# Optimization experiments

Hardware: AMD Instinct MI355X
Metric: run time of the kernel (lower is better)

Reference implementation:

```python
import jax, jax.numpy as jnp
import numpy as np

L = 19
PAD1 = L // 2          # 9 (top/left)
PAD2 = L // 2          # 9 (bottom/right, l is odd)


def setup_inputs() -> dict:
    key = jax.random.key(0)
    k1, k2 = jax.random.split(key)
    B, C, H, W = 2, 3, 256, 256
    inp = jax.random.normal(k1, (B, C, H, W), dtype=jnp.float32)
    # per-pixel blur kernels: (B, H*W, l, l), nonnegative
    kern = jax.random.uniform(k2, (B, H * W, L, L), dtype=jnp.float32)
    return {"input": inp, "kernel": kern}


def reference(input, kernel):
    B, C, H, W = input.shape
    l = L
    K2 = l * l
    # reflection pad (pad_1 left/top, pad_2 right/bottom)
    pad = jnp.pad(input, ((0, 0), (0, 0), (PAD1, PAD2), (PAD1, PAD2)), mode="reflect")
    Hp, Wp = pad.shape[-2:]
    # im2col: (B*C, 1, Hp, Wp) -> (B*C, K2, H, W); with 1 input channel the
    # patch-channel ordering is row-major over (ki, kj), matching torch.Unfold
    x = pad.reshape(B * C, 1, Hp, Wp)
    patches = jax.lax.conv_general_dilated_patches(
        x, filter_shape=(l, l), window_strides=(1, 1), padding="VALID"
    )  # (B*C, K2, H, W)
    patches = patches.reshape(B, C, K2, H * W)
    # kernel: (B, HW, l, l) -> (B, HW, K2); shared across the C=3 channels
    kflat = kernel.reshape(B, H * W, K2)
    # per-pixel weighted sum over the K2 window, then divide by l^2 (divisor_=True)
    out = jnp.einsum("bckp,bpk->bcp", patches, kflat) / jnp.float32(l * l)
    return out.reshape(B, C, H, W)
```

## Files before the change

### kernel.cpp

```cpp
#include <hip/hip_runtime.h>

#define KL   19
#define K2   361
#define W    256
#define H    256
#define HW   65536
#define C    3
#define PADL 9
#define B    2
#define TC   34
#define TPOS (KL * TC)

__global__ __launch_bounds__(256, 8) void blur_fused(
    const float* __restrict__ in,
    const float* __restrict__ kern,
    float* __restrict__ out)
{
    __shared__ float tile[TPOS * 4];

    const int tid = threadIdx.x;
    const int pb  = blockIdx.x << 4;
    const int b   = pb >> 16;
    const int i   = (pb >> 8) & 255;
    const int j0  = pb & 255;

    const float* in_b = in + (size_t)b * (C * HW);
    for (int s = tid; s < TPOS * 4; s += 256) {
        const int ch  = s & 3;
        const int pos = s >> 2;
        if (ch < 3) {
            const int r  = pos / TC;
            const int cc = pos - r * TC;
            int ro = i + r - PADL;
            ro = (ro < 0) ? -ro : ro;
            ro = (ro > H - 1) ? 2 * (H - 1) - ro : ro;
            int co = j0 + cc - PADL;
            co = (co < 0) ? -co : co;
            co = (co > W - 1) ? 2 * (W - 1) - co : co;
            tile[s] = in_b[ch * HW + ro * W + co];
        }
    }
    __syncthreads();

    const int sub = tid & 15;
    const int q   = tid >> 4;
    const int p   = pb + q;
    const float* krow = kern + (size_t)p * K2 + sub;

    float w[23];
    #pragma unroll
    for (int c = 0; c < 23; ++c) {
        const int t = sub + 16 * c;
        w[c] = (t < K2) ? krow[16 * c] : 0.f;
    }

    float a0 = 0.f, a1 = 0.f, a2 = 0.f;
    #pragma unroll
    for (int c = 0; c < 23; ++c) {
        int t = sub + 16 * c;
        if (t > K2 - 1) t = K2 - 1;
        const int ki  = t / KL;
        const int kj  = t - ki * KL;
        const int pos = ki * TC + kj + q;
        const float* src = &tile[pos * 4];
        a0 += w[c] * src[0];
        a1 += w[c] * src[1];
        a2 += w[c] * src[2];
    }

    #pragma unroll
    for (int o = 8; o >= 1; o >>= 1) {
        a0 += __shfl_xor(a0, o, 16);
        a1 += __shfl_xor(a1, o, 16);
        a2 += __shfl_xor(a2, o, 16);
    }

    if (sub == 0) {
        const float s = 1.0f / (float)K2;
        float* ob = out + (size_t)b * (C * HW) + i * W + j0 + q;
        ob[0]      = a0 * s;
        ob[HW]     = a1 * s;
        ob[2 * HW] = a2 * s;
    }
}

extern "C" void kernel_launch(void* const* d_in, const int* in_sizes, int n_in,
                              void* d_out, int out_size, void* d_ws, size_t ws_size,
                              hipStream_t stream) {
    const float* in   = (const float*)d_in[0];
    const float* kern = (const float*)d_in[1];
    float* out        = (float*)d_out;

    const int npix = B * HW;
    dim3 grid(npix / 16), block(256);
    hipLaunchKernelGGL(blur_fused, grid, block, 0, stream, in, kern, out);
}
```

Measured before the change: 38.12 us.

## Process 4x16 pixel tile per block to reuse shared input halo

Each block now covers 4 rows by 16 columns instead of a single 16-pixel row segment, loading a 22x34 halo tile once and looping over the four rows. This cuts the redundant input halo loads, since the old layout reloaded 19 rows per 16 pixels. The grid shrinks by four and each block does four times the work. The kernel weights (the dominant traffic) are still streamed once per pixel, so the gain is limited to halo traffic and fewer block launches, at the cost of fewer blocks to hide latency.

New measurement: 39.13 us. +2.7%, slower.

```diff
diff --git a/kernel.cpp b/kernel.cpp
--- a/kernel.cpp
+++ b/kernel.cpp
@@ -9,7 +9,8 @@
 #define PADL 9
 #define B    2
 #define TC   34
-#define TPOS (KL * TC)
+#define TR   22
+#define TPOS (TR * TC)
 
 __global__ __launch_bounds__(256, 8) void blur_fused(
     const float* __restrict__ in,
@@ -19,10 +20,11 @@
     __shared__ float tile[TPOS * 4];
 
     const int tid = threadIdx.x;
-    const int pb  = blockIdx.x << 4;
-    const int b   = pb >> 16;
-    const int i   = (pb >> 8) & 255;
-    const int j0  = pb & 255;
+    const int bid = blockIdx.x;
+    const int b   = bid >> 10;
+    const int rem = bid & 1023;
+    const int i0  = (rem >> 4) << 2;
+    const int j0  = (rem & 15) << 4;
 
     const float* in_b = in + (size_t)b * (C * HW);
     for (int s = tid; s < TPOS * 4; s += 256) {
@@ -31,7 +33,7 @@
         if (ch < 3) {
             const int r  = pos / TC;
             const int cc = pos - r * TC;
-            int ro = i + r - PADL;
+            int ro = i0 + r - PADL;
             ro = (ro < 0) ? -ro : ro;
             ro = (ro > H - 1) ? 2 * (H - 1) - ro : ro;
             int co = j0 + cc - PADL;
@@ -44,43 +46,46 @@
 
     const int sub = tid & 15;
     const int q   = tid >> 4;
-    const int p   = pb + q;
-    const float* krow = kern + (size_t)p * K2 + sub;
-
-    float w[23];
-    #pragma unroll
-    for (int c = 0; c < 23; ++c) {
-        const int t = sub + 16 * c;
-        w[c] = (t < K2) ? krow[16 * c] : 0.f;
-    }
-
-    float a0 = 0.f, a1 = 0.f, a2 = 0.f;
-    #pragma unroll
-    for (int c = 0; c < 23; ++c) {
-        int t = sub + 16 * c;
-        if (t > K2 - 1) t = K2 - 1;
-        const int ki  = t / KL;
-        const int kj  = t - ki * KL;
-        const int pos = ki * TC + kj + q;
-        const float* src = &tile[pos * 4];
-        a0 += w[c] * src[0];
-        a1 += w[c] * src[1];
-        a2 += w[c] * src[2];
-    }
+    const float scale = 1.0f / (float)K2;
 
     #pragma unroll
-    for (int o = 8; o >= 1; o >>= 1) {
-        a0 += __shfl_xor(a0, o, 16);
-        a1 += __shfl_xor(a1, o, 16);
-        a2 += __shfl_xor(a2, o, 16);
-    }
+    for (int r = 0; r < 4; ++r) {
+        const int p = (i0 + r) * W + j0 + q;
+        const float* krow = kern + ((size_t)b * HW + p) * K2 + sub;
 
-    if (sub == 0) {
-        const float s = 1.0f / (float)K2;
-        float* ob = out + (size_t)b * (C * HW) + i * W + j0 + q;
-        ob[0]      = a0 * s;
-        ob[HW]     = a1 * s;
-        ob[2 * HW] = a2 * s;
+        float w[23];
+        #pragma unroll
+        for (int c = 0; c < 23; ++c) {
+            const int t = sub + 16 * c;
+            w[c] = (t < K2) ? krow[16 * c] : 0.f;
+        }
+
+        float a0 = 0.f, a1 = 0.f, a2 = 0.f;
+        #pragma unroll
+        for (int c = 0; c < 23; ++c) {
+            int t = sub + 16 * c;
+            if (t > K2 - 1) t = K2 - 1;
+            const int ki = t / KL;
+            const int kj = t - ki * KL;
+            const float* src = &tile[((ki + r) * TC + kj + q) * 4];
+            a0 += w[c] * src[0];
+            a1 += w[c] * src[1];
+            a2 += w[c] * src[2];
+        }
+
+        #pragma unroll
+        for (int o = 8; o >= 1; o >>= 1) {
+            a0 += __shfl_xor(a0, o, 16);
+            a1 += __shfl_xor(a1, o, 16);
+            a2 += __shfl_xor(a2, o, 16);
+        }
+
+        if (sub == 0) {
+            float* ob = out + (size_t)b * (C * HW) + p;
+            ob[0]      = a0 * scale;
+            ob[HW]     = a1 * scale;
+            ob[2 * HW] = a2 * scale;
+        }
     }
 }
 
@@ -91,7 +96,6 @@
     const float* kern = (const float*)d_in[1];
     float* out        = (float*)d_out;
 
-    const int npix = B * HW;
-    dim3 grid(npix / 16), block(256);
+    dim3 grid(B * (H / 4) * (W / 16)), block(256);
     hipLaunchKernelGGL(blur_fused, grid, block, 0, stream, in, kern, out);
 }
```
